# Performance work log

Hardware: AMD Instinct MI355X
Metric: run time of the kernel (lower is better)

Reference implementation:

```python
import jax, jax.numpy as jnp
import numpy as np


def normalize_adj(adj):
    """Symmetrize (adj + adj.T*(adj.T>adj) - adj*(adj.T>adj)), add self loops, row-normalize D^-1 A."""
    at = jnp.swapaxes(adj, -1, -2)
    mask = (at > adj).astype(adj.dtype)
    a = adj + at * mask - adj * mask
    m = a.shape[-1]
    a = a + jnp.eye(m, dtype=a.dtype)
    rowsum = a.sum(axis=-1, keepdims=True)
    inv = jnp.where(rowsum > 0, 1.0 / rowsum, 0.0)
    return a * inv


def setup_inputs() -> dict:
    key = jax.random.key(0)
    ks = jax.random.split(key, 8)
    N, n, T, dim, M = 4, 3, 512, 2048, 256
    x = jax.random.normal(ks[0], (N, n, T, dim), dtype=jnp.float32)
    nodes = jax.random.normal(ks[1], (N, M, dim), dtype=jnp.float32)
    adj = (jax.random.uniform(ks[2], (N, M, M)) < 0.05).astype(jnp.float32)
    conv_w = jax.random.normal(ks[3], (2048, dim, 3), dtype=jnp.float32) * 0.02  # OIH
    conv_b = jnp.zeros((2048,), dtype=jnp.float32)
    W1 = jax.random.normal(ks[4], (dim, dim), dtype=jnp.float32) * 0.02
    b1 = jnp.zeros((dim,), dtype=jnp.float32)
    W2 = jax.random.normal(ks[5], (dim, dim), dtype=jnp.float32) * 0.02
    b2 = jnp.zeros((dim,), dtype=jnp.float32)
    return {"x": x, "nodes": nodes, "adj": adj, "conv_w": conv_w, "conv_b": conv_b,
            "W1": W1, "b1": b1, "W2": W2, "b2": b2}


def reference(x, nodes, adj, conv_w, conv_b, W1, b1, W2, b2):
    N, n, T, dim = x.shape
    # Conv1d front-end: (N*n, C=dim, T), kernel 3, pad 1, then ReLU
    feats = x.reshape(N * n, T, dim).transpose(0, 2, 1)  # [B, C, T]
    feats = jax.lax.conv_general_dilated(
        feats, conv_w, window_strides=(1,), padding=[(1, 1)],
        dimension_numbers=("NCH", "OIH", "NCH"))
    feats = jax.nn.relu(feats + conv_b[None, :, None])
    feats = feats.transpose(0, 2, 1).reshape(N, n, T, dim)
    # GCN_Module over per-sample node graphs (batched over N)
    a = normalize_adj(adj)                                   # [N, M, M]
    h = jax.nn.relu(jnp.einsum("bij,bjf->bif", a, nodes @ W1) + b1)
    out = jnp.einsum("bij,bjf->bif", a, h @ W2) + b2         # [N, M, dim]
    return feats, out
```

## Files before the change

### kernel.cpp

```cpp
#include <hip/hip_runtime.h>
#include <stdint.h>

typedef __bf16 bf16x8 __attribute__((ext_vector_type(8)));
typedef float floatx4 __attribute__((ext_vector_type(4)));

#define SB0 __builtin_amdgcn_sched_barrier(0)

__device__ __forceinline__ void gload_lds16(const void* g, void* l) {
    __builtin_amdgcn_global_load_lds((const __attribute__((address_space(1))) void*)g,
                                     (__attribute__((address_space(3))) void*)l, 16, 0, 0);
}

__device__ __forceinline__ uint16_t f2bf(float f) {
    uint32_t u = __float_as_uint(f);
    u += 0x7fff + ((u >> 16) & 1);
    return (uint16_t)(u >> 16);
}
__device__ __forceinline__ uint32_t f2bf2(float lo, float hi) {
    return (uint32_t)f2bf(lo) | ((uint32_t)f2bf(hi) << 16);
}

struct AmulSM {
    float vv[256];
    int   jj[256];
    float part[4];
    int   wcnt[4];
    int   woff[4];
    float sinv;
    int   n0;
};

__device__ __forceinline__ void amul_body(const float* __restrict__ adj,
                                          const float* __restrict__ H,
                                          uint16_t* __restrict__ outp,
                                          int b, int i, int tid, AmulSM* sm)
{
    const float* A = adj + ((size_t)b << 16);
    float aij = A[(i << 8) + tid];
    float aji = A[(tid << 8) + i];
    float v = fmaxf(aij, aji);
    if (tid == i) v += 1.0f;

    float s = v;
    #pragma unroll
    for (int off = 32; off > 0; off >>= 1) s += __shfl_down(s, off);

    bool pred = v != 0.0f;
    unsigned long long m = __ballot(pred);
    int wid = tid >> 6;
    if ((tid & 63) == 0) { sm->part[wid] = s; sm->wcnt[wid] = (int)__popcll(m); }
    __syncthreads();
    if (tid == 0) {
        float t = sm->part[0] + sm->part[1] + sm->part[2] + sm->part[3];
        sm->sinv = t > 0.0f ? 1.0f / t : 0.0f;
        int o = 0;
        #pragma unroll
        for (int w = 0; w < 4; ++w) { sm->woff[w] = o; o += sm->wcnt[w]; }
        sm->n0 = o;
    }
    __syncthreads();
    if (pred) {
        int pos = sm->woff[wid] + (int)__popcll(m & ((1ull << (tid & 63)) - 1ull));
        sm->vv[pos] = v * sm->sinv;
        sm->jj[pos] = tid;
    }
    __syncthreads();

    const int n0 = sm->n0;
    const int f0 = tid * 8;
    const float* Hb = H + (((size_t)b) << 8) * 2048;
    float acc[8] = {};
    for (int c = 0; c < n0; ++c) {
        float av = sm->vv[c];
        const float* hp = Hb + (size_t)sm->jj[c] * 2048 + f0;
        float4 p = *(const float4*)hp;
        float4 q = *(const float4*)(hp + 4);
        acc[0] += av * p.x; acc[1] += av * p.y; acc[2] += av * p.z; acc[3] += av * p.w;
        acc[4] += av * q.x; acc[5] += av * q.y; acc[6] += av * q.z; acc[7] += av * q.w;
    }
    uint4 o;
    o.x = f2bf2(acc[0], acc[1]);
    o.y = f2bf2(acc[2], acc[3]);
    o.z = f2bf2(acc[4], acc[5]);
    o.w = f2bf2(acc[6], acc[7]);
    *(uint4*)(outp + (((size_t)b << 8) + i) * 2048 + f0) = o;
}

__device__ __forceinline__ void amul_swizzle(int bid, int& b, int& i) {
    int x = bid & 7, g = bid >> 3;
    b = x >> 1;
    i = ((x & 1) << 7) + g;
}

#define PR_AM 1024
#define PR_W  3072
#define PR_T  5120
#define PR_N  17456

__global__ __launch_bounds__(256)
void k_prep(const float* __restrict__ x, uint16_t* __restrict__ xpad,
            const float* __restrict__ w, uint16_t* __restrict__ wT,
            const float* __restrict__ W1, const float* __restrict__ W2,
            uint16_t* __restrict__ W1T, uint16_t* __restrict__ W2T,
            const float* __restrict__ adj, const float* __restrict__ nodes,
            uint16_t* __restrict__ gbf)
{
    __shared__ union {
        float  wbuf[6144];
        float  tile[64][65];
        AmulSM am;
    } sm;
    const int bid = blockIdx.x;
    const int tid = threadIdx.x;

    if (bid < PR_AM) {
        int b, i; amul_swizzle(bid, b, i);
        amul_body(adj, nodes, gbf, b, i, tid, &sm.am);
    } else if (bid < PR_W) {
        int o = bid - PR_AM;
        const float* src = w + (size_t)o * 6144;
        uint16_t*    dst = wT + (size_t)o * 6144;
        #pragma unroll
        for (int it = 0; it < 24; ++it)
            sm.wbuf[it * 256 + tid] = src[it * 256 + tid];
        __syncthreads();
        #pragma unroll
        for (int h = 0; h < 3; ++h)
            #pragma unroll
            for (int c = 0; c < 8; ++c) {
                int i = c * 256 + tid;
                dst[h * 2048 + i] = f2bf(sm.wbuf[i * 3 + h]);
            }
    } else if (bid < PR_T) {
        int t  = bid - PR_W;
        int z  = t >> 10;
        int by = (t >> 5) & 31;
        int bx = t & 31;
        const float* src = z ? W2 : W1;
        uint16_t*    dst = z ? W2T : W1T;
        int tx = tid & 63, ty = tid >> 6;
        for (int rr = ty; rr < 64; rr += 4)
            sm.tile[rr][tx] = src[(size_t)(by * 64 + rr) * 2048 + bx * 64 + tx];
        __syncthreads();
        for (int rr = ty; rr < 64; rr += 4)
            dst[(size_t)(bx * 64 + rr) * 2048 + by * 64 + tx] = f2bf(sm.tile[tx][rr]);
    } else {
        int idx4 = (bid - PR_T) * 256 + tid;
        int ch4  = idx4 & 511;
        int tmp  = idx4 >> 9;
        int b    = tmp / 514;
        int tt   = tmp - b * 514;
        float4 v = {0.0f, 0.0f, 0.0f, 0.0f};
        if (tt >= 1 && tt <= 512)
            v = *(const float4*)(x + ((size_t)(b * 512 + tt - 1) << 11) + ch4 * 4);
        uint2 o = { f2bf2(v.x, v.y), f2bf2(v.z, v.w) };
        ((uint2*)xpad)[idx4] = o;
    }
}

template<bool RELU>
__device__ __forceinline__ void g128_tile(char* lds, const uint16_t* __restrict__ A,
                                          const uint16_t* __restrict__ BT,
                                          float* __restrict__ C, const float* __restrict__ bias,
                                          int rt, int ct, int tid)
{
    char* As = lds;
    char* Bs = lds + 16384;
    const int lane = tid & 63, wave = tid >> 6;
    const int wm = (wave >> 1) * 64, wn = (wave & 1) * 64;
    const int lm = lane & 15, lq = lane >> 4;
    const int abyte = (wm + lm) * 64 + ((lq * 16) ^ ((lm & 3) << 4));
    const int bbyte = (wn + lm) * 64 + ((lq * 16) ^ ((lm & 3) << 4));

    int soff[4];
    #pragma unroll
    for (int j = 0; j < 4; ++j) {
        int c = tid + 256 * j;
        int row = (c >> 2) & 127;
        soff[j] = row * 2048 + ((c >> 9) << 5) + (((c & 3) ^ (row & 3)) << 3);
    }

    floatx4 acc[4][4] = {};
    for (int k0 = 0; k0 < 2048; k0 += 64) {
        #pragma unroll
        for (int j = 0; j < 4; ++j) {
            gload_lds16(A  + (size_t)rt * 2048 + soff[j] + k0, As + tid * 16 + j * 4096);
            gload_lds16(BT + (size_t)ct * 2048 + soff[j] + k0, Bs + tid * 16 + j * 4096);
        }
        __syncthreads();
        #pragma unroll
        for (int s = 0; s < 2; ++s) {
            bf16x8 af[4], bfr[4];
            #pragma unroll
            for (int mt = 0; mt < 4; ++mt)
                af[mt] = *(const bf16x8*)(As + s * 8192 + abyte + mt * 1024);
            #pragma unroll
            for (int nt = 0; nt < 4; ++nt)
                bfr[nt] = *(const bf16x8*)(Bs + s * 8192 + bbyte + nt * 1024);
            #pragma unroll
            for (int mt = 0; mt < 4; ++mt)
                #pragma unroll
                for (int nt = 0; nt < 4; ++nt)
                    acc[mt][nt] = __builtin_amdgcn_mfma_f32_16x16x32_bf16(af[mt], bfr[nt], acc[mt][nt], 0, 0, 0);
        }
        __syncthreads();
    }

    #pragma unroll
    for (int mt = 0; mt < 4; ++mt)
        #pragma unroll
        for (int nt = 0; nt < 4; ++nt) {
            int col = ct + wn + nt * 16 + lm;
            float bv = bias[col];
            #pragma unroll
            for (int r = 0; r < 4; ++r) {
                int row = rt + wm + mt * 16 + lq * 4 + r;
                float v = acc[mt][nt][r] + bv;
                if (RELU) v = fmaxf(v, 0.0f);
                C[(size_t)row * 2048 + col] = v;
            }
        }
}

template<int CUR, bool STG, int VN>
__device__ __forceinline__ void conv_w2(char* smem, int tid,
    const uint16_t* (&aP)[3], const uint16_t* (&bP)[4],
    int abase, int bbase, floatx4 (&acc)[6][8])
{
    char* As  = smem + CUR * 12288;
    char* Bs  = smem + 24576 + CUR * 16384;
    char* Asn = smem + (CUR ^ 1) * 12288;
    char* Bsn = smem + 24576 + (CUR ^ 1) * 16384;

    if constexpr (STG) {
        #pragma unroll
        for (int j = 0; j < 3; ++j) { gload_lds16(aP[j], Asn + tid * 16 + j * 4096); aP[j] += 32; }
        #pragma unroll
        for (int j = 0; j < 4; ++j) { gload_lds16(bP[j], Bsn + tid * 16 + j * 4096); bP[j] += 32; }
    }
    SB0;
    asm volatile("s_waitcnt vmcnt(%0)" :: "i"(VN));
    SB0;
    __builtin_amdgcn_s_barrier();
    SB0;

    bf16x8 bv[8], av[3];
    #pragma unroll
    for (int fn = 0; fn < 8; ++fn) bv[fn] = *(const bf16x8*)(Bs + bbase + fn * 1024);
    #pragma unroll
    for (int fm = 0; fm < 3; ++fm) av[fm] = *(const bf16x8*)(As + abase + fm * 1024);
    __builtin_amdgcn_s_setprio(1);
    #pragma unroll
    for (int fm = 0; fm < 3; ++fm)
        #pragma unroll
        for (int fn = 0; fn < 8; ++fn)
            acc[fm][fn] = __builtin_amdgcn_mfma_f32_16x16x32_bf16(av[fm], bv[fn], acc[fm][fn], 0, 0, 0);
    __builtin_amdgcn_s_setprio(0);
    #pragma unroll
    for (int fm = 0; fm < 3; ++fm) av[fm] = *(const bf16x8*)(As + abase + 3072 + fm * 1024);
    __builtin_amdgcn_s_setprio(1);
    #pragma unroll
    for (int fm = 0; fm < 3; ++fm)
        #pragma unroll
        for (int fn = 0; fn < 8; ++fn)
            acc[3 + fm][fn] = __builtin_amdgcn_mfma_f32_16x16x32_bf16(av[fm], bv[fn], acc[3 + fm][fn], 0, 0, 0);
    __builtin_amdgcn_s_setprio(0);
    SB0;
    __builtin_amdgcn_s_barrier();
    SB0;
}

__global__ __launch_bounds__(256, 2)
void k_big(const uint16_t* __restrict__ xpad, const uint16_t* __restrict__ wmT,
           float* __restrict__ feats, const float* __restrict__ conv_b,
           const uint16_t* __restrict__ gbf, const uint16_t* __restrict__ W1T,
           float* __restrict__ h, const float* __restrict__ b1)
{
    __shared__ __align__(16) char smem[57344];
    const int bid = blockIdx.x;
    const int tid = threadIdx.x;

    if (bid < 256) {
        const int xcd  = bid & 7;
        const int gg   = bid >> 3;
        const int tile = xcd * 32 + gg;
        const int rt   = (tile >> 3) * 192;
        const int ct   = (tile & 7) * 256;

        const int lane = tid & 63, wave = tid >> 6;
        const int mw = wave >> 1, nw = wave & 1;
        const int lm = lane & 15, lq = lane >> 4;
        const int abase = (mw * 96 + lm) * 64 + ((lq * 16) ^ ((lm & 3) << 4));
        const int bbase = (nw * 128 + lm) * 64 + ((lq * 16) ^ ((lm & 3) << 4));

        const uint16_t* aP[3];
        const uint16_t* bP[4];
        #pragma unroll
        for (int j = 0; j < 3; ++j) {
            int c = tid + 256 * j;
            int row = c >> 2;
            int R = rt + row;
            aP[j] = xpad + (((size_t)((R >> 9) * 514 + (R & 511))) << 11)
                         + (((c & 3) ^ (row & 3)) << 3);
        }
        #pragma unroll
        for (int j = 0; j < 4; ++j) {
            int c = tid + 256 * j;
            int row = c >> 2;
            bP[j] = wmT + (size_t)(ct + row) * 6144 + (((c & 3) ^ (row & 3)) << 3);
        }

        #pragma unroll
        for (int j = 0; j < 3; ++j) { gload_lds16(aP[j], smem + tid * 16 + j * 4096); aP[j] += 32; }
        #pragma unroll
        for (int j = 0; j < 4; ++j) { gload_lds16(bP[j], smem + 24576 + tid * 16 + j * 4096); bP[j] += 32; }

        floatx4 acc[6][8] = {};
        #pragma unroll 1
        for (int it = 0; it < 95; ++it) {
            conv_w2<0, true, 7>(smem, tid, aP, bP, abase, bbase, acc);
            conv_w2<1, true, 7>(smem, tid, aP, bP, abase, bbase, acc);
        }
        conv_w2<0, true, 7>(smem, tid, aP, bP, abase, bbase, acc);
        conv_w2<1, false, 0>(smem, tid, aP, bP, abase, bbase, acc);

        #pragma unroll
        for (int fm = 0; fm < 6; ++fm)
            #pragma unroll
            for (int fn = 0; fn < 8; ++fn) {
                int col = ct + nw * 128 + fn * 16 + lm;
                float bb = conv_b[col];
                #pragma unroll
                for (int r = 0; r < 4; ++r) {
                    int row = rt + mw * 96 + fm * 16 + lq * 4 + r;
                    feats[(size_t)row * 2048 + col] = fmaxf(acc[fm][fn][r] + bb, 0.0f);
                }
            }
    } else {
        const int t   = bid - 256;
        const int idx = (t & 7) * 16 + (t >> 3);
        const int rt  = (idx & 7) * 128;
        const int ct  = (idx >> 3) * 128;
        g128_tile<true>(smem, gbf, W1T, h, b1, rt, ct, tid);
    }
}

__global__ __launch_bounds__(256)
void k_amul(const float* __restrict__ adj, const float* __restrict__ H,
            uint16_t* __restrict__ outp)
{
    __shared__ AmulSM sm;
    int b, i; amul_swizzle(blockIdx.x, b, i);
    amul_body(adj, H, outp, b, i, threadIdx.x, &sm);
}

__global__ __launch_bounds__(256)
void k_gemm64(const uint16_t* __restrict__ A, const uint16_t* __restrict__ BT,
              float* __restrict__ C, const float* __restrict__ bias)
{
    __shared__ __align__(16) char lds[32768];
    const int bid = blockIdx.x;
    const int idx = (bid & 7) * 16 + (bid >> 3);
    const int rt  = (idx & 7) * 128;
    const int ct  = (idx >> 3) * 128;
    g128_tile<false>(lds, A, BT, C, bias, rt, ct, threadIdx.x);
}


extern "C" void kernel_launch(void* const* d_in, const int* in_sizes, int n_in,
                              void* d_out, int out_size, void* d_ws, size_t ws_size,
                              hipStream_t stream)
{
    const float* x      = (const float*)d_in[0];
    const float* nodes  = (const float*)d_in[1];
    const float* adj    = (const float*)d_in[2];
    const float* conv_w = (const float*)d_in[3];
    const float* conv_b = (const float*)d_in[4];
    const float* W1     = (const float*)d_in[5];
    const float* b1     = (const float*)d_in[6];
    const float* W2     = (const float*)d_in[7];
    const float* b2     = (const float*)d_in[8];
    float* out = (float*)d_out;

    char* ws = (char*)d_ws;
    uint16_t* xpad   = (uint16_t*)(ws);
    uint16_t* wmT    = (uint16_t*)(ws + 25288704);
    uint16_t* W1T    = (uint16_t*)(ws + 50454528);
    uint16_t* W2T    = (uint16_t*)(ws + 58843136);
    uint16_t* gbf    = (uint16_t*)(ws + 67231744);
    float*    h      = (float*)   (ws + 71426048);
    uint16_t* ahb    = (uint16_t*)(ws + 79814656);

    k_prep<<<PR_N, 256, 0, stream>>>(x, xpad, conv_w, wmT,
                                     W1, W2, W1T, W2T, adj, nodes, gbf);
    k_big<<<384, 256, 0, stream>>>(xpad, wmT, out, conv_b, gbf, W1T, h, b1);
    k_amul<<<1024, 256, 0, stream>>>(adj, h, ahb);
    k_gemm64<<<128, 256, 0, stream>>>(ahb, W2T, out + 12582912, b2);
}
```

Measured before the change: 479.3 us.

## Retile conv GEMM to 256x256 blocks with 8 waves and deeper LDS pipeline

The conv implicit-GEMM moves from 192x256 tiles with 4 waves to 256x256 tiles with 8 waves (512 threads). LDS grows to 128KB and holds two k-steps per stage, so global loads are issued a full stage ahead. The loop has more barriers, with each wave computing a 128x64 sub-tile split into two halves. The W1 GEMM blocks are paired so that each 512-thread block runs two 128x128 tiles, one per half. The goal is more operand reuse per block and fewer blocks (192 instead of 256), at the cost of lower occupancy from 128KB LDS per block and extra barrier synchronisation.

```diff
diff --git a/kernel.cpp b/kernel.cpp
--- a/kernel.cpp
+++ b/kernel.cpp
@@ -222,126 +222,169 @@
         }
 }
 
-template<int CUR, bool STG, int VN>
-__device__ __forceinline__ void conv_w2(char* smem, int tid,
-    const uint16_t* (&aP)[3], const uint16_t* (&bP)[4],
-    int abase, int bbase, floatx4 (&acc)[6][8])
-{
-    char* As  = smem + CUR * 12288;
-    char* Bs  = smem + 24576 + CUR * 16384;
-    char* Asn = smem + (CUR ^ 1) * 12288;
-    char* Bsn = smem + 24576 + (CUR ^ 1) * 16384;
-
+template<int PAR, bool STG, int VN2, bool W1>
+__device__ __forceinline__ void conv_tile(char* smem, int tid,
+    const uint16_t* (&aS)[2], const uint16_t* (&bS)[2],
+    int aro, int bro, floatx4 (&acc)[8][4])
+{
+    char* A0 = smem + (PAR * 2) * 16384;
+    char* A1 = smem + (PAR * 2 + 1) * 16384;
+    char* B0 = smem + 65536 + (PAR * 2) * 16384;
+    char* B1 = smem + 65536 + (PAR * 2 + 1) * 16384;
+    char* An0 = smem + ((PAR ^ 1) * 2) * 16384;
+    char* An1 = smem + ((PAR ^ 1) * 2 + 1) * 16384;
+    char* Bn0 = smem + 65536 + ((PAR ^ 1) * 2) * 16384;
+    char* Bn1 = smem + 65536 + ((PAR ^ 1) * 2 + 1) * 16384;
+
+    bf16x8 av[4], bv[4];
+
+    #pragma unroll
+    for (int nt = 0; nt < 4; ++nt) bv[nt] = *(const bf16x8*)(B0 + bro + nt * 1024);
+    #pragma unroll
+    for (int mt = 0; mt < 4; ++mt) av[mt] = *(const bf16x8*)(A0 + aro + mt * 1024);
     if constexpr (STG) {
-        #pragma unroll
-        for (int j = 0; j < 3; ++j) { gload_lds16(aP[j], Asn + tid * 16 + j * 4096); aP[j] += 32; }
-        #pragma unroll
-        for (int j = 0; j < 4; ++j) { gload_lds16(bP[j], Bsn + tid * 16 + j * 4096); bP[j] += 32; }
-    }
-    SB0;
-    asm volatile("s_waitcnt vmcnt(%0)" :: "i"(VN));
-    SB0;
-    __builtin_amdgcn_s_barrier();
-    SB0;
-
-    bf16x8 bv[8], av[3];
-    #pragma unroll
-    for (int fn = 0; fn < 8; ++fn) bv[fn] = *(const bf16x8*)(Bs + bbase + fn * 1024);
-    #pragma unroll
-    for (int fm = 0; fm < 3; ++fm) av[fm] = *(const bf16x8*)(As + abase + fm * 1024);
+        gload_lds16(bS[0], Bn0 + tid * 16);
+        gload_lds16(bS[1], Bn0 + 8192 + tid * 16);
+        gload_lds16(aS[0], An0 + tid * 16);
+        gload_lds16(aS[1], An0 + 8192 + tid * 16);
+    }
+    SB0; __builtin_amdgcn_s_barrier();
+    asm volatile("s_waitcnt lgkmcnt(0)"); SB0;
     __builtin_amdgcn_s_setprio(1);
     #pragma unroll
-    for (int fm = 0; fm < 3; ++fm)
-        #pragma unroll
-        for (int fn = 0; fn < 8; ++fn)
-            acc[fm][fn] = __builtin_amdgcn_mfma_f32_16x16x32_bf16(av[fm], bv[fn], acc[fm][fn], 0, 0, 0);
+    for (int mt = 0; mt < 4; ++mt)
+        #pragma unroll
+        for (int nt = 0; nt < 4; ++nt)
+            acc[mt][nt] = __builtin_amdgcn_mfma_f32_16x16x32_bf16(av[mt], bv[nt], acc[mt][nt], 0, 0, 0);
     __builtin_amdgcn_s_setprio(0);
-    #pragma unroll
-    for (int fm = 0; fm < 3; ++fm) av[fm] = *(const bf16x8*)(As + abase + 3072 + fm * 1024);
+    SB0; __builtin_amdgcn_s_barrier(); SB0;
+
+    #pragma unroll
+    for (int mt = 0; mt < 4; ++mt) av[mt] = *(const bf16x8*)(A0 + aro + 4096 + mt * 1024);
+    if constexpr (STG) {
+        gload_lds16(bS[0] + 32, Bn1 + tid * 16);
+        gload_lds16(bS[1] + 32, Bn1 + 8192 + tid * 16);
+        gload_lds16(aS[0] + 32, An1 + tid * 16);
+        gload_lds16(aS[1] + 32, An1 + 8192 + tid * 16);
+        aS[0] += 64; aS[1] += 64; bS[0] += 64; bS[1] += 64;
+    }
+    SB0; __builtin_amdgcn_s_barrier();
+    asm volatile("s_waitcnt lgkmcnt(0)"); SB0;
     __builtin_amdgcn_s_setprio(1);
     #pragma unroll
-    for (int fm = 0; fm < 3; ++fm)
-        #pragma unroll
-        for (int fn = 0; fn < 8; ++fn)
-            acc[3 + fm][fn] = __builtin_amdgcn_mfma_f32_16x16x32_bf16(av[fm], bv[fn], acc[3 + fm][fn], 0, 0, 0);
+    for (int mt = 0; mt < 4; ++mt)
+        #pragma unroll
+        for (int nt = 0; nt < 4; ++nt)
+            acc[4 + mt][nt] = __builtin_amdgcn_mfma_f32_16x16x32_bf16(av[mt], bv[nt], acc[4 + mt][nt], 0, 0, 0);
     __builtin_amdgcn_s_setprio(0);
-    SB0;
-    __builtin_amdgcn_s_barrier();
-    SB0;
-}
-
-__global__ __launch_bounds__(256, 2)
+    asm volatile("s_waitcnt vmcnt(%0)" :: "i"(VN2));
+    SB0; __builtin_amdgcn_s_barrier(); SB0;
+
+    #pragma unroll
+    for (int nt = 0; nt < 4; ++nt) bv[nt] = *(const bf16x8*)(B1 + bro + nt * 1024);
+    #pragma unroll
+    for (int mt = 0; mt < 4; ++mt) av[mt] = *(const bf16x8*)(A1 + aro + mt * 1024);
+    SB0; __builtin_amdgcn_s_barrier();
+    asm volatile("s_waitcnt lgkmcnt(0)"); SB0;
+    __builtin_amdgcn_s_setprio(1);
+    #pragma unroll
+    for (int mt = 0; mt < 4; ++mt)
+        #pragma unroll
+        for (int nt = 0; nt < 4; ++nt)
+            acc[mt][nt] = __builtin_amdgcn_mfma_f32_16x16x32_bf16(av[mt], bv[nt], acc[mt][nt], 0, 0, 0);
+    __builtin_amdgcn_s_setprio(0);
+    SB0; __builtin_amdgcn_s_barrier(); SB0;
+
+    #pragma unroll
+    for (int mt = 0; mt < 4; ++mt) av[mt] = *(const bf16x8*)(A1 + aro + 4096 + mt * 1024);
+    SB0; __builtin_amdgcn_s_barrier();
+    asm volatile("s_waitcnt lgkmcnt(0)"); SB0;
+    __builtin_amdgcn_s_setprio(1);
+    #pragma unroll
+    for (int mt = 0; mt < 4; ++mt)
+        #pragma unroll
+        for (int nt = 0; nt < 4; ++nt)
+            acc[4 + mt][nt] = __builtin_amdgcn_mfma_f32_16x16x32_bf16(av[mt], bv[nt], acc[4 + mt][nt], 0, 0, 0);
+    __builtin_amdgcn_s_setprio(0);
+    if constexpr (W1) asm volatile("s_waitcnt vmcnt(4)");
+    SB0; __builtin_amdgcn_s_barrier(); SB0;
+}
+
+__global__ __launch_bounds__(512, 2)
 void k_big(const uint16_t* __restrict__ xpad, const uint16_t* __restrict__ wmT,
            float* __restrict__ feats, const float* __restrict__ conv_b,
            const uint16_t* __restrict__ gbf, const uint16_t* __restrict__ W1T,
            float* __restrict__ h, const float* __restrict__ b1)
 {
-    __shared__ __align__(16) char smem[57344];
+    __shared__ __align__(16) char smem[131072];
     const int bid = blockIdx.x;
     const int tid = threadIdx.x;
 
-    if (bid < 256) {
-        const int xcd  = bid & 7;
-        const int gg   = bid >> 3;
-        const int tile = xcd * 32 + gg;
-        const int rt   = (tile >> 3) * 192;
-        const int ct   = (tile & 7) * 256;
+    if (bid < 192) {
+        const int xcd = bid & 7;
+        const int g   = bid >> 3;
+        const int rt  = g * 256;
+        const int ct  = xcd * 256;
 
         const int lane = tid & 63, wave = tid >> 6;
-        const int mw = wave >> 1, nw = wave & 1;
+        const int mw = wave >> 2, nw = wave & 3;
         const int lm = lane & 15, lq = lane >> 4;
-        const int abase = (mw * 96 + lm) * 64 + ((lq * 16) ^ ((lm & 3) << 4));
-        const int bbase = (nw * 128 + lm) * 64 + ((lq * 16) ^ ((lm & 3) << 4));
-
-        const uint16_t* aP[3];
-        const uint16_t* bP[4];
-        #pragma unroll
-        for (int j = 0; j < 3; ++j) {
-            int c = tid + 256 * j;
-            int row = c >> 2;
-            int R = rt + row;
-            aP[j] = xpad + (((size_t)((R >> 9) * 514 + (R & 511))) << 11)
-                         + (((c & 3) ^ (row & 3)) << 3);
+        const int rxor = (lq * 16) ^ ((lm & 3) << 4);
+        const int aro = (mw * 128 + lm) * 64 + rxor;
+        const int bro = (nw * 64 + lm) * 64 + rxor;
+
+        const uint16_t* aS[2];
+        const uint16_t* bS[2];
+        const int srow = tid >> 2;
+        const int scol = ((tid & 3) ^ (srow & 3)) << 3;
+        #pragma unroll
+        for (int j = 0; j < 2; ++j) {
+            int R = rt + j * 128 + srow;
+            aS[j] = xpad + (((size_t)((R >> 9) * 514 + (R & 511))) << 11) + scol;
+            bS[j] = wmT + (size_t)(ct + j * 128 + srow) * 6144 + scol;
         }
-        #pragma unroll
-        for (int j = 0; j < 4; ++j) {
-            int c = tid + 256 * j;
-            int row = c >> 2;
-            bP[j] = wmT + (size_t)(ct + row) * 6144 + (((c & 3) ^ (row & 3)) << 3);
+
+        gload_lds16(bS[0], smem + 65536 + tid * 16);
+        gload_lds16(bS[1], smem + 65536 + 8192 + tid * 16);
+        gload_lds16(aS[0], smem + tid * 16);
+        gload_lds16(aS[1], smem + 8192 + tid * 16);
+        gload_lds16(bS[0] + 32, smem + 65536 + 16384 + tid * 16);
+        gload_lds16(bS[1] + 32, smem + 65536 + 16384 + 8192 + tid * 16);
+        gload_lds16(aS[0] + 32, smem + 16384 + tid * 16);
+        gload_lds16(aS[1] + 32, smem + 16384 + 8192 + tid * 16);
+        aS[0] += 64; aS[1] += 64; bS[0] += 64; bS[1] += 64;
+        asm volatile("s_waitcnt vmcnt(4)");
+        SB0; __builtin_amdgcn_s_barrier(); SB0;
+
+        floatx4 acc[8][4] = {};
+        #pragma unroll 1
+        for (int it = 0; it < 47; ++it) {
+            conv_tile<0, true, 8, true>(smem, tid, aS, bS, aro, bro, acc);
+            conv_tile<1, true, 8, true>(smem, tid, aS, bS, aro, bro, acc);
         }
-
-        #pragma unroll
-        for (int j = 0; j < 3; ++j) { gload_lds16(aP[j], smem + tid * 16 + j * 4096); aP[j] += 32; }
-        #pragma unroll
-        for (int j = 0; j < 4; ++j) { gload_lds16(bP[j], smem + 24576 + tid * 16 + j * 4096); bP[j] += 32; }
-
-        floatx4 acc[6][8] = {};
-        #pragma unroll 1
-        for (int it = 0; it < 95; ++it) {
-            conv_w2<0, true, 7>(smem, tid, aP, bP, abase, bbase, acc);
-            conv_w2<1, true, 7>(smem, tid, aP, bP, abase, bbase, acc);
-        }
-        conv_w2<0, true, 7>(smem, tid, aP, bP, abase, bbase, acc);
-        conv_w2<1, false, 0>(smem, tid, aP, bP, abase, bbase, acc);
-
-        #pragma unroll
-        for (int fm = 0; fm < 6; ++fm)
-            #pragma unroll
-            for (int fn = 0; fn < 8; ++fn) {
-                int col = ct + nw * 128 + fn * 16 + lm;
+        conv_tile<0, true, 8, true >(smem, tid, aS, bS, aro, bro, acc);
+        conv_tile<1, false, 0, false>(smem, tid, aS, bS, aro, bro, acc);
+
+        #pragma unroll
+        for (int mt = 0; mt < 8; ++mt)
+            #pragma unroll
+            for (int nt = 0; nt < 4; ++nt) {
+                int col = ct + nw * 64 + nt * 16 + lm;
                 float bb = conv_b[col];
                 #pragma unroll
                 for (int r = 0; r < 4; ++r) {
-                    int row = rt + mw * 96 + fm * 16 + lq * 4 + r;
-                    feats[(size_t)row * 2048 + col] = fmaxf(acc[fm][fn][r] + bb, 0.0f);
+                    int row = rt + mw * 128 + mt * 16 + lq * 4 + r;
+                    feats[(size_t)row * 2048 + col] = fmaxf(acc[mt][nt][r] + bb, 0.0f);
                 }
             }
     } else {
-        const int t   = bid - 256;
-        const int idx = (t & 7) * 16 + (t >> 3);
-        const int rt  = (idx & 7) * 128;
-        const int ct  = (idx >> 3) * 128;
-        g128_tile<true>(smem, gbf, W1T, h, b1, rt, ct, tid);
+        const int t    = bid - 192;
+        const int half = tid >> 8;
+        const int st   = t * 2 + half;
+        const int idx  = (st & 7) * 16 + (st >> 3);
+        const int rt   = (idx & 7) * 128;
+        const int ct   = (idx >> 3) * 128;
+        g128_tile<true>(smem + half * 32768, gbf, W1T, h, b1, rt, ct, tid & 255);
     }
 }
 
@@ -393,7 +436,7 @@
 
     k_prep<<<PR_N, 256, 0, stream>>>(x, xpad, conv_w, wmT,
                                      W1, W2, W1T, W2T, adj, nodes, gbf);
-    k_big<<<384, 256, 0, stream>>>(xpad, wmT, out, conv_b, gbf, W1T, h, b1);
+    k_big<<<256, 512, 0, stream>>>(xpad, wmT, out, conv_b, gbf, W1T, h, b1);
     k_amul<<<1024, 256, 0, stream>>>(adj, h, ahb);
     k_gemm64<<<128, 256, 0, stream>>>(ahb, W2T, out + 12582912, b2);
 }
```

Measured after the change: 436.4 us. -8.9%, faster.

## Restructure conv GEMM to 512-thread blocks, 32x32 MFMA and 4-stage LDS pipeline

Applied to the files above, without the earlier changes.

The conv front-end GEMM now runs on 8-wave blocks using 32x32x16 bf16 MFMA instead of 16x16x32. Each wave computes a 96x64 sub-tile. The K loop uses a four-buffer LDS ring with loads issued three steps ahead, replacing the double buffer, so global-to-LDS latency overlaps more compute. The GCN W1 GEMM blocks are repacked so each 512-thread block computes two 128x128 tiles, which cuts the grid to 320 blocks. The cost is twice the shared memory per block (112 KB), which likely limits each CU to one resident block, plus a changed epilogue layout for the 32x32 accumulators.

```diff
diff --git a/kernel.cpp b/kernel.cpp
--- a/kernel.cpp
+++ b/kernel.cpp
@@ -3,6 +3,7 @@
 
 typedef __bf16 bf16x8 __attribute__((ext_vector_type(8)));
 typedef float floatx4 __attribute__((ext_vector_type(4)));
+typedef float floatx16 __attribute__((ext_vector_type(16)));
 
 #define SB0 __builtin_amdgcn_sched_barrier(0)
 
@@ -222,61 +223,65 @@
         }
 }
 
-template<int CUR, bool STG, int VN>
-__device__ __forceinline__ void conv_w2(char* smem, int tid,
-    const uint16_t* (&aP)[3], const uint16_t* (&bP)[4],
-    int abase, int bbase, floatx4 (&acc)[6][8])
-{
-    char* As  = smem + CUR * 12288;
-    char* Bs  = smem + 24576 + CUR * 16384;
-    char* Asn = smem + (CUR ^ 1) * 12288;
-    char* Bsn = smem + 24576 + (CUR ^ 1) * 16384;
+template<int BUF, bool STG, int VN>
+__device__ __forceinline__ void conv_win(char* ldsb, int tid,
+    const uint16_t*& aS0, const uint16_t*& aS1,
+    const uint16_t*& bS0, const uint16_t*& bS1,
+    const int (&arow)[3], const int (&brow)[2], const int (&kso)[2],
+    floatx16 (&acc)[3][2])
+{
+    char* As  = ldsb + BUF * 12288;
+    char* Bs  = ldsb + 49152 + BUF * 16384;
+    constexpr int NB = (BUF + 3) & 3;
+    char* As3 = ldsb + NB * 12288;
+    char* Bs3 = ldsb + 49152 + NB * 16384;
+
+    bf16x8 av[3][2], bv[2][2];
+    #pragma unroll
+    for (int fm = 0; fm < 3; ++fm)
+        #pragma unroll
+        for (int s = 0; s < 2; ++s)
+            av[fm][s] = *(const bf16x8*)(As + arow[fm] + kso[s]);
+    #pragma unroll
+    for (int fn = 0; fn < 2; ++fn)
+        #pragma unroll
+        for (int s = 0; s < 2; ++s)
+            bv[fn][s] = *(const bf16x8*)(Bs + brow[fn] + kso[s]);
 
     if constexpr (STG) {
-        #pragma unroll
-        for (int j = 0; j < 3; ++j) { gload_lds16(aP[j], Asn + tid * 16 + j * 4096); aP[j] += 32; }
-        #pragma unroll
-        for (int j = 0; j < 4; ++j) { gload_lds16(bP[j], Bsn + tid * 16 + j * 4096); bP[j] += 32; }
+        gload_lds16(aS0, As3 + tid * 16); aS0 += 32;
+        if (tid < 256) { gload_lds16(aS1, As3 + 8192 + tid * 16); aS1 += 32; }
+        gload_lds16(bS0, Bs3 + tid * 16); bS0 += 32;
+        gload_lds16(bS1, Bs3 + 8192 + tid * 16); bS1 += 32;
     }
     SB0;
-    asm volatile("s_waitcnt vmcnt(%0)" :: "i"(VN));
+    __builtin_amdgcn_s_barrier();
+    asm volatile("s_waitcnt lgkmcnt(0)");
+    SB0;
+    __builtin_amdgcn_s_setprio(1);
+    #pragma unroll
+    for (int fm = 0; fm < 3; ++fm)
+        #pragma unroll
+        for (int fn = 0; fn < 2; ++fn)
+            #pragma unroll
+            for (int s = 0; s < 2; ++s)
+                acc[fm][fn] = __builtin_amdgcn_mfma_f32_32x32x16_bf16(
+                    av[fm][s], bv[fn][s], acc[fm][fn], 0, 0, 0);
+    __builtin_amdgcn_s_setprio(0);
+    SB0;
+    if constexpr (VN >= 0) asm volatile("s_waitcnt vmcnt(%0)" :: "i"(VN));
     SB0;
     __builtin_amdgcn_s_barrier();
     SB0;
-
-    bf16x8 bv[8], av[3];
-    #pragma unroll
-    for (int fn = 0; fn < 8; ++fn) bv[fn] = *(const bf16x8*)(Bs + bbase + fn * 1024);
-    #pragma unroll
-    for (int fm = 0; fm < 3; ++fm) av[fm] = *(const bf16x8*)(As + abase + fm * 1024);
-    __builtin_amdgcn_s_setprio(1);
-    #pragma unroll
-    for (int fm = 0; fm < 3; ++fm)
-        #pragma unroll
-        for (int fn = 0; fn < 8; ++fn)
-            acc[fm][fn] = __builtin_amdgcn_mfma_f32_16x16x32_bf16(av[fm], bv[fn], acc[fm][fn], 0, 0, 0);
-    __builtin_amdgcn_s_setprio(0);
-    #pragma unroll
-    for (int fm = 0; fm < 3; ++fm) av[fm] = *(const bf16x8*)(As + abase + 3072 + fm * 1024);
-    __builtin_amdgcn_s_setprio(1);
-    #pragma unroll
-    for (int fm = 0; fm < 3; ++fm)
-        #pragma unroll
-        for (int fn = 0; fn < 8; ++fn)
-            acc[3 + fm][fn] = __builtin_amdgcn_mfma_f32_16x16x32_bf16(av[fm], bv[fn], acc[3 + fm][fn], 0, 0, 0);
-    __builtin_amdgcn_s_setprio(0);
-    SB0;
-    __builtin_amdgcn_s_barrier();
-    SB0;
-}
-
-__global__ __launch_bounds__(256, 2)
+}
+
+__global__ __launch_bounds__(512, 2)
 void k_big(const uint16_t* __restrict__ xpad, const uint16_t* __restrict__ wmT,
            float* __restrict__ feats, const float* __restrict__ conv_b,
            const uint16_t* __restrict__ gbf, const uint16_t* __restrict__ W1T,
            float* __restrict__ h, const float* __restrict__ b1)
 {
-    __shared__ __align__(16) char smem[57344];
+    __shared__ __align__(16) char smem[114688];
     const int bid = blockIdx.x;
     const int tid = threadIdx.x;
 
@@ -288,60 +293,78 @@
         const int ct   = (tile & 7) * 256;
 
         const int lane = tid & 63, wave = tid >> 6;
-        const int mw = wave >> 1, nw = wave & 1;
-        const int lm = lane & 15, lq = lane >> 4;
-        const int abase = (mw * 96 + lm) * 64 + ((lq * 16) ^ ((lm & 3) << 4));
-        const int bbase = (nw * 128 + lm) * 64 + ((lq * 16) ^ ((lm & 3) << 4));
-
-        const uint16_t* aP[3];
-        const uint16_t* bP[4];
-        #pragma unroll
-        for (int j = 0; j < 3; ++j) {
-            int c = tid + 256 * j;
-            int row = c >> 2;
-            int R = rt + row;
-            aP[j] = xpad + (((size_t)((R >> 9) * 514 + (R & 511))) << 11)
-                         + (((c & 3) ^ (row & 3)) << 3);
+        const int mw = wave >> 2, nw = wave & 3;
+        const int l31 = lane & 31;
+        const int lk  = (lane >> 5) * 16;
+        const int xv  = (l31 & 3) << 4;
+        int arow[3], brow[2], kso[2];
+        kso[0] = lk ^ xv;
+        kso[1] = (32 + lk) ^ xv;
+        #pragma unroll
+        for (int fm = 0; fm < 3; ++fm) arow[fm] = (mw * 96 + fm * 32 + l31) * 64;
+        #pragma unroll
+        for (int fn = 0; fn < 2; ++fn) brow[fn] = (nw * 64 + fn * 32 + l31) * 64;
+
+        const int c1  = 512 + tid;
+        const int r0  = tid >> 2,  kc0 = ((tid & 3) ^ (r0 & 3)) * 8;
+        const int r1  = c1 >> 2,   kc1 = ((c1 & 3) ^ (r1 & 3)) * 8;
+
+        const int RA0 = rt + r0;
+        const int RA1 = rt + r1;
+        const uint16_t* aS0 = xpad + (((size_t)((RA0 >> 9) * 514 + (RA0 & 511))) << 11) + kc0;
+        const uint16_t* aS1 = xpad + (((size_t)((RA1 >> 9) * 514 + (RA1 & 511))) << 11) + kc1;
+        const uint16_t* bS0 = wmT + (size_t)(ct + r0) * 6144 + kc0;
+        const uint16_t* bS1 = wmT + (size_t)(ct + r1) * 6144 + kc1;
+
+        #pragma unroll
+        for (int p = 0; p < 3; ++p) {
+            char* As3 = smem + p * 12288;
+            char* Bs3 = smem + 49152 + p * 16384;
+            gload_lds16(aS0, As3 + tid * 16); aS0 += 32;
+            if (tid < 256) { gload_lds16(aS1, As3 + 8192 + tid * 16); aS1 += 32; }
+            gload_lds16(bS0, Bs3 + tid * 16); bS0 += 32;
+            gload_lds16(bS1, Bs3 + 8192 + tid * 16); bS1 += 32;
         }
-        #pragma unroll
-        for (int j = 0; j < 4; ++j) {
-            int c = tid + 256 * j;
-            int row = c >> 2;
-            bP[j] = wmT + (size_t)(ct + row) * 6144 + (((c & 3) ^ (row & 3)) << 3);
+        SB0;
+        asm volatile("s_waitcnt vmcnt(6)");
+        SB0;
+        __builtin_amdgcn_s_barrier();
+        SB0;
+
+        floatx16 acc[3][2] = {};
+        #pragma unroll 1
+        for (int it = 0; it < 47; ++it) {
+            conv_win<0, true, 6>(smem, tid, aS0, aS1, bS0, bS1, arow, brow, kso, acc);
+            conv_win<1, true, 6>(smem, tid, aS0, aS1, bS0, bS1, arow, brow, kso, acc);
+            conv_win<2, true, 6>(smem, tid, aS0, aS1, bS0, bS1, arow, brow, kso, acc);
+            conv_win<3, true, 6>(smem, tid, aS0, aS1, bS0, bS1, arow, brow, kso, acc);
         }
-
-        #pragma unroll
-        for (int j = 0; j < 3; ++j) { gload_lds16(aP[j], smem + tid * 16 + j * 4096); aP[j] += 32; }
-        #pragma unroll
-        for (int j = 0; j < 4; ++j) { gload_lds16(bP[j], smem + 24576 + tid * 16 + j * 4096); bP[j] += 32; }
-
-        floatx4 acc[6][8] = {};
-        #pragma unroll 1
-        for (int it = 0; it < 95; ++it) {
-            conv_w2<0, true, 7>(smem, tid, aP, bP, abase, bbase, acc);
-            conv_w2<1, true, 7>(smem, tid, aP, bP, abase, bbase, acc);
-        }
-        conv_w2<0, true, 7>(smem, tid, aP, bP, abase, bbase, acc);
-        conv_w2<1, false, 0>(smem, tid, aP, bP, abase, bbase, acc);
-
-        #pragma unroll
-        for (int fm = 0; fm < 6; ++fm)
-            #pragma unroll
-            for (int fn = 0; fn < 8; ++fn) {
-                int col = ct + nw * 128 + fn * 16 + lm;
+        conv_win<0, true,  6>(smem, tid, aS0, aS1, bS0, bS1, arow, brow, kso, acc);
+        conv_win<1, false, 3>(smem, tid, aS0, aS1, bS0, bS1, arow, brow, kso, acc);
+        conv_win<2, false, 0>(smem, tid, aS0, aS1, bS0, bS1, arow, brow, kso, acc);
+        conv_win<3, false,-1>(smem, tid, aS0, aS1, bS0, bS1, arow, brow, kso, acc);
+
+        const int rhi = (lane >> 5) * 4;
+        #pragma unroll
+        for (int fm = 0; fm < 3; ++fm)
+            #pragma unroll
+            for (int fn = 0; fn < 2; ++fn) {
+                int col = ct + nw * 64 + fn * 32 + l31;
                 float bb = conv_b[col];
                 #pragma unroll
-                for (int r = 0; r < 4; ++r) {
-                    int row = rt + mw * 96 + fm * 16 + lq * 4 + r;
+                for (int r = 0; r < 16; ++r) {
+                    int row = rt + mw * 96 + fm * 32 + (r & 3) + 8 * (r >> 2) + rhi;
                     feats[(size_t)row * 2048 + col] = fmaxf(acc[fm][fn][r] + bb, 0.0f);
                 }
             }
     } else {
-        const int t   = bid - 256;
-        const int idx = (t & 7) * 16 + (t >> 3);
-        const int rt  = (idx & 7) * 128;
-        const int ct  = (idx >> 3) * 128;
-        g128_tile<true>(smem, gbf, W1T, h, b1, rt, ct, tid);
+        const int t    = bid - 256;
+        const int half = tid >> 8;
+        const int st   = t * 2 + half;
+        const int idx  = (st & 7) * 16 + (st >> 3);
+        const int rt   = (idx & 7) * 128;
+        const int ct   = (idx >> 3) * 128;
+        g128_tile<true>(smem + half * 32768, gbf, W1T, h, b1, rt, ct, tid & 255);
     }
 }
 
@@ -393,7 +416,7 @@
 
     k_prep<<<PR_N, 256, 0, stream>>>(x, xpad, conv_w, wmT,
                                      W1, W2, W1T, W2T, adj, nodes, gbf);
-    k_big<<<384, 256, 0, stream>>>(xpad, wmT, out, conv_b, gbf, W1T, h, b1);
+    k_big<<<320, 512, 0, stream>>>(xpad, wmT, out, conv_b, gbf, W1T, h, b1);
     k_amul<<<1024, 256, 0, stream>>>(adj, h, ahb);
     k_gemm64<<<128, 256, 0, stream>>>(ahb, W2T, out + 12582912, b2);
 }
```

After: 462.7 us. -3.5%, faster.
